# Performance work log

Measured on AMD Instinct MI355X. Metric: run time of the kernel, lower is better.

The kernel has to match this reference:

```python
import jax, jax.numpy as jnp
import numpy as np

B = 65536      # batch
IN = 784       # 1*28*28 flattened input
H = 768        # hidden_size
D = 3          # num_domains
E = 64         # expert hidden
C = 10         # classes
EPS = 1e-5     # BatchNorm eps


def setup_inputs() -> dict:
    key = jax.random.key(0)
    ks = jax.random.split(key, 8)
    s = lambda k, shp, sc: (jax.random.normal(k, shp, jnp.float32) * sc)
    return dict(
        x=jax.random.normal(ks[0], (B, 1, 28, 28), jnp.float32),
        # pre_classifier: Linear(784, H) + BatchNorm1d(H) affine params
        W1=s(ks[1], (IN, H), 0.03), b1=jnp.zeros((H,), jnp.float32),
        gamma=jnp.ones((H,), jnp.float32), beta=jnp.zeros((H,), jnp.float32),
        # discriminator: Linear(H,H) -> ReLU -> Linear(H,D)
        Wd1=s(ks[2], (H, H), 0.03), bd1=jnp.zeros((H,), jnp.float32),
        Wd2=s(ks[3], (H, D), 0.03), bd2=jnp.zeros((D,), jnp.float32),
        # per-domain expert classifiers: Linear(H,64) -> ReLU -> Linear(64,10), stacked over D
        Wa=s(ks[4], (D, H, E), 0.03), ba=jnp.zeros((D, E), jnp.float32),
        Wb=s(ks[5], (D, E, C), 0.1), bb=jnp.zeros((D, C), jnp.float32),
    )


def reference(x, W1, b1, gamma, beta, Wd1, bd1, Wd2, bd2, Wa, ba, Wb, bb):
    xf = x.reshape(x.shape[0], -1)                      # [B, 784]
    h = xf @ W1 + b1                                    # [B, H]
    # BatchNorm1d in training mode: batch mean / biased variance
    mu = h.mean(axis=0)
    var = jnp.mean((h - mu) ** 2, axis=0)
    feat = jax.nn.relu((h - mu) / jnp.sqrt(var + EPS) * gamma + beta)  # [B, H]
    # ReverseLayerF with alpha=0: identity forward, zero gradient back to feat
    rev = jax.lax.stop_gradient(feat)
    dom_out = jax.nn.relu(rev @ Wd1 + bd1) @ Wd2 + bd2  # [B, D]
    dom_pred = jnp.argmax(dom_out, axis=1)              # [B] int routing
    # hard routing: compute all D tiny experts densely, select by dom_pred
    hid = jax.nn.relu(jnp.einsum('bh,dhe->bde', feat, Wa) + ba)   # [B, D, E]
    all_out = jnp.einsum('bde,dec->bdc', hid, Wb) + bb            # [B, D, C]
    outs = jnp.take_along_axis(all_out, dom_pred[:, None, None], axis=1)[:, 0, :]  # [B, C]
    return outs, dom_out
```

## Files before the change

### kernel.cpp

```cpp
#include <hip/hip_runtime.h>
#include <math.h>

#define BATCH 65536
#define KIN   784
#define HD    768
#define FCAP  16384

typedef float f32x4 __attribute__((ext_vector_type(4)));
typedef short s16x8 __attribute__((ext_vector_type(8)));
typedef unsigned int __attribute__((address_space(3))) lds_u32;
typedef const unsigned int __attribute__((address_space(1))) glb_u32;

__device__ __forceinline__ float frelu(float x){ return x > 0.f ? x : 0.f; }

__device__ __forceinline__ unsigned int cvtpk(float a, float b){
    unsigned int r;
    asm("v_cvt_pk_bf16_f32 %0, %1, %2" : "=v"(r) : "v"(a), "v"(b));
    return r;
}
__device__ __forceinline__ unsigned short f2bf(float v){
    unsigned int u = __builtin_bit_cast(unsigned int, v);
    u += 0x7FFFu + ((u >> 16) & 1u);
    return (unsigned short)(u >> 16);
}
__device__ __forceinline__ float bf2f(unsigned short s){
    unsigned int u = ((unsigned int)s) << 16;
    return __builtin_bit_cast(float, u);
}
__device__ __forceinline__ void gload16(const void* g, void* l){
    __builtin_amdgcn_global_load_lds((glb_u32*)g, (lds_u32*)l, 16, 0, 0);
}

__global__ __launch_bounds__(256)
void cvtX(const float* __restrict__ x, unsigned short* __restrict__ xbf)
{
    int idx = blockIdx.x * 256 + threadIdx.x;
    int row = idx / 104, c = (idx - row * 104) * 8;
    uint4 o = make_uint4(0, 0, 0, 0);
    if (c < KIN) {
        const float* p = x + (size_t)row * KIN + c;
        float4 a = *(const float4*)p;
        float4 b = *(const float4*)(p + 4);
        o.x = cvtpk(a.x, a.y); o.y = cvtpk(a.z, a.w);
        o.z = cvtpk(b.x, b.y); o.w = cvtpk(b.z, b.w);
    }
    *(uint4*)(xbf + (size_t)row * 832 + c) = o;
}

__global__ __launch_bounds__(256)
void featBN(const unsigned short* __restrict__ hbf,
            const float* __restrict__ scale, const float* __restrict__ shift,
            unsigned short* __restrict__ fbf)
{
    int idx = blockIdx.x * 256 + threadIdx.x;
    int row = idx / 96, c = (idx - row * 96) * 8;
    s16x8 hv = *(const s16x8*)(hbf + (size_t)row * HD + c);
    float4 s0 = *(const float4*)(scale + c), s1 = *(const float4*)(scale + c + 4);
    float4 t0 = *(const float4*)(shift + c), t1 = *(const float4*)(shift + c + 4);
    float v[8];
    v[0] = frelu(bf2f((unsigned short)hv[0]) * s0.x + t0.x);
    v[1] = frelu(bf2f((unsigned short)hv[1]) * s0.y + t0.y);
    v[2] = frelu(bf2f((unsigned short)hv[2]) * s0.z + t0.z);
    v[3] = frelu(bf2f((unsigned short)hv[3]) * s0.w + t0.w);
    v[4] = frelu(bf2f((unsigned short)hv[4]) * s1.x + t1.x);
    v[5] = frelu(bf2f((unsigned short)hv[5]) * s1.y + t1.y);
    v[6] = frelu(bf2f((unsigned short)hv[6]) * s1.z + t1.z);
    v[7] = frelu(bf2f((unsigned short)hv[7]) * s1.w + t1.w);
    uint4 o;
    o.x = cvtpk(v[0], v[1]); o.y = cvtpk(v[2], v[3]);
    o.z = cvtpk(v[4], v[5]); o.w = cvtpk(v[6], v[7]);
    *(uint4*)(fbf + (size_t)row * HD + c) = o;
}

__global__ __launch_bounds__(256)
void tileW(const float* __restrict__ W, char* __restrict__ Wh, char* __restrict__ Wl,
           int K, int N, int NT)
{
    int chunk = blockIdx.x;
    int nb = chunk / NT, t = chunk - nb * NT;
    int tid = threadIdx.x;
    #pragma unroll
    for (int q = 0; q < 2; q++) {
        int idx = q * 256 + tid;
        int r = idx >> 2, p = idx & 3;
        int s = (p ^ ((r >> 1) & 3)) & 3;
        int kb = t * 32 + s * 8;
        int n = nb * 128 + r;
        s16x8 hv, lv;
        #pragma unroll
        for (int e = 0; e < 8; e++) {
            int k = kb + e;
            float v = (k < K) ? W[(size_t)k * N + n] : 0.f;
            unsigned short h = f2bf(v);
            hv[e] = (short)h;
            lv[e] = (short)f2bf(v - bf2f(h));
        }
        *(s16x8*)(Wh + (size_t)chunk * 8192 + idx * 16) = hv;
        *(s16x8*)(Wl + (size_t)chunk * 8192 + idx * 16) = lv;
    }
}

__global__ __launch_bounds__(256)
void tileWa(const float* __restrict__ Wa, char* __restrict__ WaC)
{
    int chunk = blockIdx.x;
    int d = chunk / 24, t = chunk - d * 24;
    int idx = threadIdx.x;
    int r = idx >> 2, p = idx & 3;
    int s = (p ^ ((r >> 1) & 3)) & 3;
    int kb = t * 32 + s * 8;
    s16x8 hv;
    #pragma unroll
    for (int e = 0; e < 8; e++)
        hv[e] = (short)f2bf(Wa[((size_t)d * HD + kb + e) * 64 + r]);
    *(s16x8*)(WaC + (size_t)chunk * 4096 + idx * 16) = hv;
}

template<int MODE>
__global__ __launch_bounds__(256, 3)
void gemm97(const unsigned short* __restrict__ Abf,
            const char* __restrict__ BhC,
            const float* __restrict__ bias,
            unsigned short* __restrict__ Hbf,
            const float* __restrict__ Wd2, double* __restrict__ domacc,
            float* __restrict__ sp1, float* __restrict__ sp2,
            int KP, int NT)
{
    __shared__ __align__(16) char sm[32768];

    int bid = blockIdx.x;
    int wg = (bid & 7) * 384 + (bid >> 3);
    int mb = wg / 6, nb = wg - mb * 6;
    int m0 = mb << 7, n0 = nb << 7;

    int tid = threadIdx.x;
    int lane = tid & 63, wid = tid >> 6;
    int wr = wid >> 1, wc = wid & 1;
    int l15 = lane & 15, l4 = lane >> 4;

    int aoff[4], boff[4];
    #pragma unroll
    for (int f = 0; f < 4; f++) {
        int ra = wr * 64 + f * 16 + l15;
        aoff[f] = ra * 64 + (((l4 ^ (ra >> 1)) & 3) << 4);
        int rb = wc * 64 + f * 16 + l15;
        boff[f] = rb * 64 + (((l4 ^ (rb >> 1)) & 3) << 4);
    }

    int ar[2], asl[2];
    #pragma unroll
    for (int q = 0; q < 2; q++) {
        int idx = q * 256 + tid;
        int r = idx >> 2, p = idx & 3;
        asl[q] = (p ^ ((r >> 1) & 3)) & 3;
        ar[q] = r;
    }

    f32x4 acc[4][4];
    #pragma unroll
    for (int i = 0; i < 4; i++)
        #pragma unroll
        for (int j = 0; j < 4; j++) acc[i][j] = (f32x4){0.f, 0.f, 0.f, 0.f};

    int NTc = 2 * NT;
    for (int t = 0; t < NT; t++) {
        int t2 = 2 * t;
        #pragma unroll
        for (int h = 0; h < 2; h++) {
            #pragma unroll
            for (int q = 0; q < 2; q++) {
                const unsigned short* src = Abf + (size_t)(m0 + ar[q]) * KP
                                          + (t2 + h) * 32 + asl[q] * 8;
                gload16(src, sm + h * 8192 + (q * 256 + tid) * 16);
            }
        }
        #pragma unroll
        for (int h = 0; h < 2; h++) {
            size_t cb = (size_t)(nb * NTc + t2 + h) * 8192;
            #pragma unroll
            for (int q = 0; q < 2; q++) {
                int off = (q * 256 + tid) * 16;
                gload16(BhC + cb + off, sm + 16384 + h * 8192 + off);
            }
        }
        __syncthreads();
        #pragma unroll
        for (int h = 0; h < 2; h++) {
            const char* ab  = sm + h * 8192;
            const char* bb2 = sm + 16384 + h * 8192;
            s16x8 fah[4], fbh[4];
            #pragma unroll
            for (int f = 0; f < 4; f++) {
                fah[f] = *(const s16x8*)(ab + aoff[f]);
                fbh[f] = *(const s16x8*)(bb2 + boff[f]);
            }
            #pragma unroll
            for (int i = 0; i < 4; i++)
                #pragma unroll
                for (int j = 0; j < 4; j++)
                    acc[i][j] = __builtin_amdgcn_mfma_f32_16x16x32_bf16(fah[i], fbh[j], acc[i][j], 0, 0, 0);
        }
        __syncthreads();
    }

    if (MODE == 0) {
        float bc[4];
        #pragma unroll
        for (int f = 0; f < 4; f++) bc[f] = bias[n0 + wc * 64 + f * 16 + l15];
        float cs[4] = {0.f,0.f,0.f,0.f}, cq[4] = {0.f,0.f,0.f,0.f};
        #pragma unroll
        for (int i = 0; i < 4; i++) {
            int rowb = m0 + wr * 64 + i * 16 + l4 * 4;
            #pragma unroll
            for (int j2 = 0; j2 < 4; j2++) {
                unsigned short* hrow = Hbf + (size_t)(rowb + j2) * HD + n0 + wc * 64 + l15;
                #pragma unroll
                for (int f = 0; f < 4; f++) {
                    float v = acc[i][f][j2] + bc[f];
                    hrow[f * 16] = (unsigned short)cvtpk(v, v);
                    cs[f] += v; cq[f] += v * v;
                }
            }
        }
        #pragma unroll
        for (int m = 16; m < 64; m <<= 1)
            #pragma unroll
            for (int f = 0; f < 4; f++) {
                cs[f] += __shfl_xor(cs[f], m, 64);
                cq[f] += __shfl_xor(cq[f], m, 64);
            }
        if (l4 == 0) {
            #pragma unroll
            for (int f = 0; f < 4; f++) {
                int col = n0 + wc * 64 + f * 16 + l15;
                sp1[(size_t)col * 1024 + mb * 2 + wr] = cs[f];
                sp2[(size_t)col * 1024 + mb * 2 + wr] = cq[f];
            }
        }
    } else {
        float bc[4], w2[4][3];
        #pragma unroll
        for (int f = 0; f < 4; f++) {
            int col = n0 + wc * 64 + f * 16 + l15;
            bc[f] = bias[col];
            w2[f][0] = Wd2[col * 3 + 0]; w2[f][1] = Wd2[col * 3 + 1]; w2[f][2] = Wd2[col * 3 + 2];
        }
        float s0[16], s1[16], s2[16];
        #pragma unroll
        for (int i = 0; i < 16; i++) { s0[i] = 0.f; s1[i] = 0.f; s2[i] = 0.f; }
        #pragma unroll
        for (int i = 0; i < 4; i++)
            #pragma unroll
            for (int j2 = 0; j2 < 4; j2++) {
                int idx = i * 4 + j2;
                #pragma unroll
                for (int f = 0; f < 4; f++) {
                    float v = frelu(acc[i][f][j2] + bc[f]);
                    s0[idx] += v * w2[f][0];
                    s1[idx] += v * w2[f][1];
                    s2[idx] += v * w2[f][2];
                }
            }
        #pragma unroll
        for (int m = 1; m < 16; m <<= 1) {
            #pragma unroll
            for (int i = 0; i < 16; i++) {
                s0[i] += __shfl_xor(s0[i], m, 64);
                s1[i] += __shfl_xor(s1[i], m, 64);
                s2[i] += __shfl_xor(s2[i], m, 64);
            }
        }
        if (l15 == 0) {
            #pragma unroll
            for (int i = 0; i < 16; i++) {
                int row = m0 + wr * 64 + (i >> 2) * 16 + l4 * 4 + (i & 3);
                atomicAdd(&domacc[(size_t)row * 3 + 0], (double)s0[i]);
                atomicAdd(&domacc[(size_t)row * 3 + 1], (double)s1[i]);
                atomicAdd(&domacc[(size_t)row * 3 + 2], (double)s2[i]);
            }
        }
    }
}

__global__ __launch_bounds__(256)
void bnfinal(const float* __restrict__ sp1, const float* __restrict__ sp2,
             const float* __restrict__ gamma, const float* __restrict__ beta,
             float* __restrict__ scale, float* __restrict__ shift)
{
    int c = blockIdx.x, t = threadIdx.x;
    const float* p1 = sp1 + (size_t)c * 1024;
    const float* p2 = sp2 + (size_t)c * 1024;
    double S = (double)p1[t] + (double)p1[t + 256] + (double)p1[t + 512] + (double)p1[t + 768];
    double Q = (double)p2[t] + (double)p2[t + 256] + (double)p2[t + 512] + (double)p2[t + 768];
    #pragma unroll
    for (int m = 1; m < 64; m <<= 1) { S += __shfl_xor(S, m, 64); Q += __shfl_xor(Q, m, 64); }
    __shared__ double sd1[4], sd2[4];
    int w = t >> 6;
    if ((t & 63) == 0) { sd1[w] = S; sd2[w] = Q; }
    __syncthreads();
    if (t == 0) {
        double Sa = sd1[0] + sd1[1] + sd1[2] + sd1[3];
        double Qa = sd2[0] + sd2[1] + sd2[2] + sd2[3];
        double mu  = Sa * (1.0 / 65536.0);
        double var = Qa * (1.0 / 65536.0) - mu * mu;
        double inv = 1.0 / sqrt(var + 1e-5);
        double sc  = inv * (double)gamma[c];
        double sh  = (double)beta[c] - mu * sc;
        scale[c] = (float)sc;
        shift[c] = (float)sh;
    }
}

__global__ __launch_bounds__(256)
void domfinal_a(const double* __restrict__ domacc, const float* __restrict__ bd2,
                float* __restrict__ outdom, int* __restrict__ fixmeta, int* __restrict__ fixlist)
{
    int r = blockIdx.x * 256 + threadIdx.x;
    double v0 = domacc[(size_t)r * 3 + 0] + (double)bd2[0];
    double v1 = domacc[(size_t)r * 3 + 1] + (double)bd2[1];
    double v2 = domacc[(size_t)r * 3 + 2] + (double)bd2[2];
    outdom[(size_t)r * 3 + 0] = (float)v0;
    outdom[(size_t)r * 3 + 1] = (float)v1;
    outdom[(size_t)r * 3 + 2] = (float)v2;
    double mx01 = v0 > v1 ? v0 : v1, mn01 = v0 > v1 ? v1 : v0;
    double best = mx01 > v2 ? mx01 : v2;
    double m2   = mx01 > v2 ? (mn01 > v2 ? mn01 : v2) : mx01;
    if (best - m2 < 1.5e-2) {
        int p = atomicAdd(fixmeta, 1);
        fixlist[p] = r;
    }
}

__global__ __launch_bounds__(256)
void gfix1(const int* __restrict__ fixmeta, const int* __restrict__ fixlist,
           const float* __restrict__ x,
           const char* __restrict__ BhC, const char* __restrict__ BlC,
           const float* __restrict__ b1, const float* __restrict__ scale,
           const float* __restrict__ shift,
           unsigned short* __restrict__ ffh, unsigned short* __restrict__ ffl)
{
    __shared__ __align__(16) char sm[32768];
    __shared__ int rowidx[128];
    int nfix = fixmeta[0]; if (nfix > FCAP) nfix = FCAP;
    int start = blockIdx.x * 128;
    if (start >= nfix) return;
    int nb = blockIdx.y;
    int n0 = nb << 7;

    int tid = threadIdx.x;
    int lane = tid & 63, wid = tid >> 6;
    int wr = wid >> 1, wc = wid & 1;
    int l15 = lane & 15, l4 = lane >> 4;

    if (tid < 128) {
        int i = start + tid;
        rowidx[tid] = fixlist[i < nfix ? i : nfix - 1];
    }
    __syncthreads();

    int aoff[4], boff[4];
    #pragma unroll
    for (int f = 0; f < 4; f++) {
        int ra = wr * 64 + f * 16 + l15;
        aoff[f] = ra * 64 + (((l4 ^ (ra >> 1)) & 3) << 4);
        int rb = wc * 64 + f * 16 + l15;
        boff[f] = rb * 64 + (((l4 ^ (rb >> 1)) & 3) << 4);
    }
    int ar[2], asl[2], arow[2];
    #pragma unroll
    for (int q = 0; q < 2; q++) {
        int idx = q * 256 + tid;
        int r = idx >> 2, p = idx & 3;
        asl[q] = (p ^ ((r >> 1) & 3)) & 3;
        ar[q] = r;
        arow[q] = rowidx[r];
    }

    f32x4 acc[4][4];
    #pragma unroll
    for (int i = 0; i < 4; i++)
        #pragma unroll
        for (int j = 0; j < 4; j++) acc[i][j] = (f32x4){0.f, 0.f, 0.f, 0.f};

    float av[2][8];
    auto loadA = [&](int t) {
        #pragma unroll
        for (int q = 0; q < 2; q++) {
            int kb = t * 32 + asl[q] * 8;
            const float* src = x + (size_t)arow[q] * KIN + kb;
            if (kb + 7 < KIN) {
                *(float4*)&av[q][0] = *(const float4*)src;
                *(float4*)&av[q][4] = *(const float4*)(src + 4);
            } else {
                #pragma unroll
                for (int e = 0; e < 8; e++) av[q][e] = (kb + e < KIN) ? src[e] : 0.f;
            }
        }
    };
    auto writeA = [&]() {
        #pragma unroll
        for (int q = 0; q < 2; q++) {
            int idx = q * 256 + tid;
            float* v = av[q];
            uint4 oh;
            oh.x = cvtpk(v[0], v[1]); oh.y = cvtpk(v[2], v[3]);
            oh.z = cvtpk(v[4], v[5]); oh.w = cvtpk(v[6], v[7]);
            float h0 = bf2f((unsigned short)(oh.x & 0xFFFF));
            float h1 = bf2f((unsigned short)(oh.x >> 16));
            float h2 = bf2f((unsigned short)(oh.y & 0xFFFF));
            float h3 = bf2f((unsigned short)(oh.y >> 16));
            float h4 = bf2f((unsigned short)(oh.z & 0xFFFF));
            float h5 = bf2f((unsigned short)(oh.z >> 16));
            float h6 = bf2f((unsigned short)(oh.w & 0xFFFF));
            float h7 = bf2f((unsigned short)(oh.w >> 16));
            uint4 ol;
            ol.x = cvtpk(v[0] - h0, v[1] - h1); ol.y = cvtpk(v[2] - h2, v[3] - h3);
            ol.z = cvtpk(v[4] - h4, v[5] - h5); ol.w = cvtpk(v[6] - h6, v[7] - h7);
            *(uint4*)(sm + idx * 16) = oh;
            *(uint4*)(sm + 8192 + idx * 16) = ol;
        }
    };

    loadA(0);
    const int NTc = 26;
    for (int t = 0; t < NTc; t++) {
        __syncthreads();
        size_t cb = (size_t)(nb * NTc + t) * 8192;
        #pragma unroll
        for (int q = 0; q < 2; q++) {
            int off = (q * 256 + tid) * 16;
            gload16(BhC + cb + off, sm + 16384 + off);
            gload16(BlC + cb + off, sm + 24576 + off);
        }
        writeA();
        if (t + 1 < NTc) loadA(t + 1);
        __syncthreads();
        s16x8 fah[4], fal[4], fbh[4], fbl[4];
        #pragma unroll
        for (int f = 0; f < 4; f++) {
            fah[f] = *(const s16x8*)(sm + aoff[f]);
            fal[f] = *(const s16x8*)(sm + 8192 + aoff[f]);
            fbh[f] = *(const s16x8*)(sm + 16384 + boff[f]);
            fbl[f] = *(const s16x8*)(sm + 24576 + boff[f]);
        }
        #pragma unroll
        for (int i = 0; i < 4; i++)
            #pragma unroll
            for (int j = 0; j < 4; j++) {
                acc[i][j] = __builtin_amdgcn_mfma_f32_16x16x32_bf16(fah[i], fbl[j], acc[i][j], 0, 0, 0);
                acc[i][j] = __builtin_amdgcn_mfma_f32_16x16x32_bf16(fal[i], fbh[j], acc[i][j], 0, 0, 0);
                acc[i][j] = __builtin_amdgcn_mfma_f32_16x16x32_bf16(fah[i], fbh[j], acc[i][j], 0, 0, 0);
            }
    }

    float bc[4], sc[4], sh[4];
    #pragma unroll
    for (int f = 0; f < 4; f++) {
        int col = n0 + wc * 64 + f * 16 + l15;
        bc[f] = b1[col]; sc[f] = scale[col]; sh[f] = shift[col];
    }
    #pragma unroll
    for (int i = 0; i < 4; i++) {
        #pragma unroll
        for (int j2 = 0; j2 < 4; j2++) {
            int pos = start + wr * 64 + i * 16 + l4 * 4 + j2;
            if (pos < nfix) {
                #pragma unroll
                for (int f = 0; f < 4; f++) {
                    int col = n0 + wc * 64 + f * 16 + l15;
                    float fl = frelu((acc[i][f][j2] + bc[f]) * sc[f] + sh[f]);
                    unsigned short hi = (unsigned short)cvtpk(fl, fl);
                    unsigned short lo = (unsigned short)cvtpk(fl - bf2f(hi), 0.f);
                    ffh[(size_t)pos * HD + col] = hi;
                    ffl[(size_t)pos * HD + col] = lo;
                }
            }
        }
    }
}

__global__ __launch_bounds__(256)
void gfix2(const int* __restrict__ fixmeta,
           const unsigned short* __restrict__ ffh, const unsigned short* __restrict__ ffl,
           const char* __restrict__ BhC, const char* __restrict__ BlC,
           const float* __restrict__ bd1, const float* __restrict__ Wd2,
           double* __restrict__ domfix)
{
    __shared__ __align__(16) char sm[32768];
    int nfix = fixmeta[0]; if (nfix > FCAP) nfix = FCAP;
    int start = blockIdx.x * 128;
    if (start >= nfix) return;
    int nb = blockIdx.y;
    int n0 = nb << 7;

    int tid = threadIdx.x;
    int lane = tid & 63, wid = tid >> 6;
    int wr = wid >> 1, wc = wid & 1;
    int l15 = lane & 15, l4 = lane >> 4;

    int aoff[4], boff[4];
    #pragma unroll
    for (int f = 0; f < 4; f++) {
        int ra = wr * 64 + f * 16 + l15;
        aoff[f] = ra * 64 + (((l4 ^ (ra >> 1)) & 3) << 4);
        int rb = wc * 64 + f * 16 + l15;
        boff[f] = rb * 64 + (((l4 ^ (rb >> 1)) & 3) << 4);
    }
    int arow[2], asl[2];
    #pragma unroll
    for (int q = 0; q < 2; q++) {
        int idx = q * 256 + tid;
        int r = idx >> 2, p = idx & 3;
        asl[q] = (p ^ ((r >> 1) & 3)) & 3;
        int pos = start + r;
        arow[q] = pos < nfix ? pos : nfix - 1;
    }

    f32x4 acc[4][4];
    #pragma unroll
    for (int i = 0; i < 4; i++)
        #pragma unroll
        for (int j = 0; j < 4; j++) acc[i][j] = (f32x4){0.f, 0.f, 0.f, 0.f};

    const int NTc = 24;
    for (int t = 0; t < NTc; t++) {
        #pragma unroll
        for (int q = 0; q < 2; q++) {
            size_t ao = (size_t)arow[q] * HD + t * 32 + asl[q] * 8;
            gload16(ffh + ao, sm + (q * 256 + tid) * 16);
            gload16(ffl + ao, sm + 8192 + (q * 256 + tid) * 16);
        }
        size_t cb = (size_t)(nb * NTc + t) * 8192;
        #pragma unroll
        for (int q = 0; q < 2; q++) {
            int off = (q * 256 + tid) * 16;
            gload16(BhC + cb + off, sm + 16384 + off);
            gload16(BlC + cb + off, sm + 24576 + off);
        }
        __syncthreads();
        s16x8 fah[4], fal[4], fbh[4], fbl[4];
        #pragma unroll
        for (int f = 0; f < 4; f++) {
            fah[f] = *(const s16x8*)(sm + aoff[f]);
            fal[f] = *(const s16x8*)(sm + 8192 + aoff[f]);
            fbh[f] = *(const s16x8*)(sm + 16384 + boff[f]);
            fbl[f] = *(const s16x8*)(sm + 24576 + boff[f]);
        }
        #pragma unroll
        for (int i = 0; i < 4; i++)
            #pragma unroll
            for (int j = 0; j < 4; j++) {
                acc[i][j] = __builtin_amdgcn_mfma_f32_16x16x32_bf16(fah[i], fbl[j], acc[i][j], 0, 0, 0);
                acc[i][j] = __builtin_amdgcn_mfma_f32_16x16x32_bf16(fal[i], fbh[j], acc[i][j], 0, 0, 0);
                acc[i][j] = __builtin_amdgcn_mfma_f32_16x16x32_bf16(fah[i], fbh[j], acc[i][j], 0, 0, 0);
            }
        __syncthreads();
    }

    float bc[4], w2[4][3];
    #pragma unroll
    for (int f = 0; f < 4; f++) {
        int col = n0 + wc * 64 + f * 16 + l15;
        bc[f] = bd1[col];
        w2[f][0] = Wd2[col * 3 + 0]; w2[f][1] = Wd2[col * 3 + 1]; w2[f][2] = Wd2[col * 3 + 2];
    }
    float s0[16], s1[16], s2[16];
    #pragma unroll
    for (int i = 0; i < 16; i++) { s0[i] = 0.f; s1[i] = 0.f; s2[i] = 0.f; }
    #pragma unroll
    for (int i = 0; i < 4; i++)
        #pragma unroll
        for (int j2 = 0; j2 < 4; j2++) {
            int idx = i * 4 + j2;
            #pragma unroll
            for (int f = 0; f < 4; f++) {
                float v = frelu(acc[i][f][j2] + bc[f]);
                s0[idx] += v * w2[f][0];
                s1[idx] += v * w2[f][1];
                s2[idx] += v * w2[f][2];
            }
        }
    #pragma unroll
    for (int m = 1; m < 16; m <<= 1) {
        #pragma unroll
        for (int i = 0; i < 16; i++) {
            s0[i] += __shfl_xor(s0[i], m, 64);
            s1[i] += __shfl_xor(s1[i], m, 64);
            s2[i] += __shfl_xor(s2[i], m, 64);
        }
    }
    if (l15 == 0) {
        #pragma unroll
        for (int i = 0; i < 16; i++) {
            int pos = start + wr * 64 + (i >> 2) * 16 + l4 * 4 + (i & 3);
            if (pos < nfix) {
                atomicAdd(&domfix[(size_t)pos * 3 + 0], (double)s0[i]);
                atomicAdd(&domfix[(size_t)pos * 3 + 1], (double)s1[i]);
                atomicAdd(&domfix[(size_t)pos * 3 + 2], (double)s2[i]);
            }
        }
    }
}

__global__ __launch_bounds__(256)
void fixfin(const int* __restrict__ fixmeta, const int* __restrict__ fixlist,
            const double* __restrict__ domfix, const float* __restrict__ bd2,
            float* __restrict__ outdom)
{
    int nfix = fixmeta[0]; if (nfix > FCAP) nfix = FCAP;
    int i = blockIdx.x * 256 + threadIdx.x;
    if (i < nfix) {
        int row = fixlist[i];
        outdom[(size_t)row * 3 + 0] = (float)(domfix[(size_t)i * 3 + 0] + (double)bd2[0]);
        outdom[(size_t)row * 3 + 1] = (float)(domfix[(size_t)i * 3 + 1] + (double)bd2[1]);
        outdom[(size_t)row * 3 + 2] = (float)(domfix[(size_t)i * 3 + 2] + (double)bd2[2]);
    }
}

__global__ __launch_bounds__(256)
void domfinal_b(const float* __restrict__ outdom, int* __restrict__ cnt, int* __restrict__ lists)
{
    __shared__ int lcnt[3], base[3];
    int tid = threadIdx.x;
    if (tid < 3) lcnt[tid] = 0;
    __syncthreads();
    int r = blockIdx.x * 256 + tid;
    float v0 = outdom[(size_t)r * 3 + 0];
    float v1 = outdom[(size_t)r * 3 + 1];
    float v2 = outdom[(size_t)r * 3 + 2];
    int p = 0; float best = v0;
    if (v1 > best) { best = v1; p = 1; }
    if (v2 > best) { best = v2; p = 2; }
    int lpos = atomicAdd(&lcnt[p], 1);
    __syncthreads();
    if (tid < 3) base[tid] = atomicAdd(&cnt[tid], lcnt[tid]);
    __syncthreads();
    lists[(size_t)p * BATCH + base[p] + lpos] = r;
}

__global__ __launch_bounds__(256)
void expert_mfma(const unsigned short* __restrict__ fbf,
                 const char* __restrict__ WaC,
                 const int* __restrict__ cnt, const int* __restrict__ lists,
                 const float* __restrict__ ba,
                 const float* __restrict__ Wb, const float* __restrict__ bb,
                 float* __restrict__ outs)
{
    __shared__ __align__(16) char sm[12288];
    __shared__ float hid[128][66];
    __shared__ int rowidx[128];

    int d = blockIdx.y;
    int count = cnt[d];
    int start = blockIdx.x * 128;
    if (start >= count) return;
    int nrows = count - start; if (nrows > 128) nrows = 128;

    int tid = threadIdx.x;
    int lane = tid & 63, wid = tid >> 6;
    int l15 = lane & 15, l4 = lane >> 4;

    if (tid < 128) {
        int i = tid < nrows ? tid : nrows - 1;
        rowidx[tid] = lists[(size_t)d * BATCH + start + i];
    }
    __syncthreads();

    int asl[2], arow[2];
    #pragma unroll
    for (int q = 0; q < 2; q++) {
        int idx = q * 256 + tid;
        int r = idx >> 2, p = idx & 3;
        asl[q] = (p ^ ((r >> 1) & 3)) & 3;
        arow[q] = rowidx[r];
    }

    int aoff[2], boff[4];
    #pragma unroll
    for (int i2 = 0; i2 < 2; i2++) {
        int ra = wid * 32 + i2 * 16 + l15;
        aoff[i2] = ra * 64 + (((l4 ^ (ra >> 1)) & 3) << 4);
    }
    #pragma unroll
    for (int f = 0; f < 4; f++) {
        int rb = f * 16 + l15;
        boff[f] = rb * 64 + (((l4 ^ (rb >> 1)) & 3) << 4);
    }

    f32x4 acc[2][4];
    #pragma unroll
    for (int i = 0; i < 2; i++)
        #pragma unroll
        for (int j = 0; j < 4; j++) acc[i][j] = (f32x4){0.f, 0.f, 0.f, 0.f};

    for (int t = 0; t < 24; t++) {
        #pragma unroll
        for (int q = 0; q < 2; q++)
            gload16(fbf + (size_t)arow[q] * HD + t * 32 + asl[q] * 8,
                    sm + (q * 256 + tid) * 16);
        gload16(WaC + (size_t)(d * 24 + t) * 4096 + tid * 16, sm + 8192 + tid * 16);
        __syncthreads();
        s16x8 fa[2], fb[4];
        #pragma unroll
        for (int i2 = 0; i2 < 2; i2++) fa[i2] = *(const s16x8*)(sm + aoff[i2]);
        #pragma unroll
        for (int f = 0; f < 4; f++)    fb[f]  = *(const s16x8*)(sm + 8192 + boff[f]);
        #pragma unroll
        for (int i2 = 0; i2 < 2; i2++)
            #pragma unroll
            for (int f = 0; f < 4; f++)
                acc[i2][f] = __builtin_amdgcn_mfma_f32_16x16x32_bf16(fa[i2], fb[f], acc[i2][f], 0, 0, 0);
        __syncthreads();
    }

    #pragma unroll
    for (int i2 = 0; i2 < 2; i2++)
        #pragma unroll
        for (int f = 0; f < 4; f++) {
            int col = f * 16 + l15;
            float bav = ba[d * 64 + col];
            #pragma unroll
            for (int j = 0; j < 4; j++) {
                int row = wid * 32 + i2 * 16 + l4 * 4 + j;
                hid[row][col] = frelu(acc[i2][f][j] + bav);
            }
        }
    __syncthreads();

    for (int o = tid; o < 1280; o += 256) {
        int r2 = o / 10, c = o - r2 * 10;
        if (r2 < nrows) {
            float s = 0.f;
            #pragma unroll 16
            for (int l = 0; l < 64; l++) s += hid[r2][l] * Wb[((size_t)d * 64 + l) * 10 + c];
            outs[(size_t)rowidx[r2] * 10 + c] = s + bb[d * 10 + c];
        }
    }
}

extern "C" void kernel_launch(void* const* d_in, const int* in_sizes, int n_in,
                              void* d_out, int out_size, void* d_ws, size_t ws_size,
                              hipStream_t stream)
{
    const float* x     = (const float*)d_in[0];
    const float* W1    = (const float*)d_in[1];
    const float* b1    = (const float*)d_in[2];
    const float* gamma = (const float*)d_in[3];
    const float* beta  = (const float*)d_in[4];
    const float* Wd1   = (const float*)d_in[5];
    const float* bd1   = (const float*)d_in[6];
    const float* Wd2   = (const float*)d_in[7];
    const float* bd2   = (const float*)d_in[8];
    const float* Wa    = (const float*)d_in[9];
    const float* ba    = (const float*)d_in[10];
    const float* Wb    = (const float*)d_in[11];
    const float* bb    = (const float*)d_in[12];

    float* out    = (float*)d_out;
    float* outs   = out;
    float* outdom = out + (size_t)BATCH * 10;

    const int NT1 = 13, NT2 = 12;
    const int NTC1 = 26, NTC2 = 24;

    char* ws = (char*)d_ws;
    size_t off = 0;
    unsigned short* hbf = (unsigned short*)(ws + off); off += (size_t)BATCH * HD * 2;
    unsigned short* xbf = (unsigned short*)(ws + off); off += (size_t)BATCH * 832 * 2;
    unsigned short* fbf = xbf;
    unsigned short* ffh = hbf;
    unsigned short* ffl = hbf + (size_t)FCAP * HD;
    char*  W1hC   = ws + off;            off += (size_t)6 * NTC1 * 8192;
    char*  W1loC  = ws + off;            off += (size_t)6 * NTC1 * 8192;
    char*  Wd1hC  = ws + off;            off += (size_t)6 * NTC2 * 8192;
    char*  Wd1loC = ws + off;            off += (size_t)6 * NTC2 * 8192;
    char*  WaC    = ws + off;            off += (size_t)3 * 24 * 4096;
    float* sp1    = (float*)(ws + off);  off += (size_t)HD * 1024 * 4;
    float* sp2    = (float*)(ws + off);  off += (size_t)HD * 1024 * 4;
    float* scale  = (float*)(ws + off);  off += HD * 4;
    float* shift  = (float*)(ws + off);  off += HD * 4;
    size_t zoff = off;
    double* domacc = (double*)(ws + off); off += (size_t)BATCH * 3 * 8;
    double* domfix = (double*)(ws + off); off += (size_t)FCAP * 3 * 8;
    int*    cnt    = (int*)(ws + off);    off += 64;
    int*    fixmeta= (int*)(ws + off);    off += 64;
    size_t zbytes = off - zoff;
    int*    lists  = (int*)(ws + off);    off += (size_t)3 * BATCH * 4;
    int*    fixlist= (int*)(ws + off);    off += (size_t)BATCH * 4;

    hipMemsetAsync(ws + zoff, 0, zbytes, stream);

    tileW<<<6 * NTC1, 256, 0, stream>>>(W1, W1hC, W1loC, KIN, HD, NTC1);
    tileW<<<6 * NTC2, 256, 0, stream>>>(Wd1, Wd1hC, Wd1loC, HD, HD, NTC2);
    tileWa<<<72, 256, 0, stream>>>(Wa, WaC);
    cvtX<<<BATCH * 104 / 256, 256, 0, stream>>>(x, xbf);

    gemm97<0><<<3072, 256, 0, stream>>>(xbf, W1hC, b1, hbf,
                                        nullptr, nullptr, sp1, sp2, 832, NT1);
    bnfinal<<<HD, 256, 0, stream>>>(sp1, sp2, gamma, beta, scale, shift);
    featBN<<<BATCH * 96 / 256, 256, 0, stream>>>(hbf, scale, shift, fbf);
    gemm97<1><<<3072, 256, 0, stream>>>(fbf, Wd1hC, bd1, nullptr,
                                        Wd2, domacc, nullptr, nullptr, HD, NT2);
    domfinal_a<<<BATCH / 256, 256, 0, stream>>>(domacc, bd2, outdom, fixmeta, fixlist);
    {
        dim3 fg(FCAP / 128, 6);
        gfix1<<<fg, 256, 0, stream>>>(fixmeta, fixlist, x, W1hC, W1loC,
                                      b1, scale, shift, ffh, ffl);
        gfix2<<<fg, 256, 0, stream>>>(fixmeta, ffh, ffl, Wd1hC, Wd1loC,
                                      bd1, Wd2, domfix);
        fixfin<<<FCAP / 256, 256, 0, stream>>>(fixmeta, fixlist, domfix, bd2, outdom);
    }
    domfinal_b<<<BATCH / 256, 256, 0, stream>>>(outdom, cnt, lists);
    dim3 eg(512, 3);
    expert_mfma<<<eg, 256, 0, stream>>>(fbf, WaC, cnt, lists, ba, Wb, bb, outs);
}
```

Baseline: 573.2 us.

## Widen GEMM block tile to 128x256 with 8 waves sharing the A tile

Both main GEMM launches now use 512-thread blocks covering 128 rows by 256 columns, instead of 256-thread blocks covering 128x128. The A tile loaded into LDS is shared across two 128-column B chunks, which halves global A traffic and the number of blocks. LDS per block grows to 48KB and the min-blocks-per-CU hint is dropped. This can lower occupancy and change register allocation. The epilogue must stay consistent with the new wave-to-column mapping.

Result: slower. 589.3 us (+2.8%).

```diff
diff --git a/kernel.cpp b/kernel.cpp
--- a/kernel.cpp
+++ b/kernel.cpp
@@ -117,7 +117,7 @@
 }
 
 template<int MODE>
-__global__ __launch_bounds__(256, 3)
+__global__ __launch_bounds__(512)
 void gemm97(const unsigned short* __restrict__ Abf,
             const char* __restrict__ BhC,
             const float* __restrict__ bias,
@@ -126,16 +126,16 @@
             float* __restrict__ sp1, float* __restrict__ sp2,
             int KP, int NT)
 {
-    __shared__ __align__(16) char sm[32768];
+    __shared__ __align__(16) char sm[49152];
 
     int bid = blockIdx.x;
-    int wg = (bid & 7) * 384 + (bid >> 3);
-    int mb = wg / 6, nb = wg - mb * 6;
-    int m0 = mb << 7, n0 = nb << 7;
+    int wg = (bid & 7) * 192 + (bid >> 3);
+    int mb = wg / 3, ct = wg - mb * 3;
+    int m0 = mb << 7, n0 = ct << 8;
 
     int tid = threadIdx.x;
     int lane = tid & 63, wid = tid >> 6;
-    int wr = wid >> 1, wc = wid & 1;
+    int wr = wid >> 2, wc = wid & 3;
     int l15 = lane & 15, l4 = lane >> 4;
 
     int aoff[4], boff[4];
@@ -143,17 +143,16 @@
     for (int f = 0; f < 4; f++) {
         int ra = wr * 64 + f * 16 + l15;
         aoff[f] = ra * 64 + (((l4 ^ (ra >> 1)) & 3) << 4);
-        int rb = wc * 64 + f * 16 + l15;
-        boff[f] = rb * 64 + (((l4 ^ (rb >> 1)) & 3) << 4);
-    }
-
-    int ar[2], asl[2];
-    #pragma unroll
-    for (int q = 0; q < 2; q++) {
-        int idx = q * 256 + tid;
-        int r = idx >> 2, p = idx & 3;
-        asl[q] = (p ^ ((r >> 1) & 3)) & 3;
-        ar[q] = r;
+        int cc = wc >> 1, sub = wc & 1;
+        int rb = sub * 64 + f * 16 + l15;
+        boff[f] = cc * 8192 + rb * 64 + (((l4 ^ (rb >> 1)) & 3) << 4);
+    }
+
+    int ar, asl;
+    {
+        int r = tid >> 2, p = tid & 3;
+        asl = (p ^ ((r >> 1) & 3)) & 3;
+        ar = r;
     }
 
     f32x4 acc[4][4];
@@ -167,27 +166,23 @@
         int t2 = 2 * t;
         #pragma unroll
         for (int h = 0; h < 2; h++) {
-            #pragma unroll
-            for (int q = 0; q < 2; q++) {
-                const unsigned short* src = Abf + (size_t)(m0 + ar[q]) * KP
-                                          + (t2 + h) * 32 + asl[q] * 8;
-                gload16(src, sm + h * 8192 + (q * 256 + tid) * 16);
-            }
-        }
-        #pragma unroll
-        for (int h = 0; h < 2; h++) {
-            size_t cb = (size_t)(nb * NTc + t2 + h) * 8192;
-            #pragma unroll
-            for (int q = 0; q < 2; q++) {
-                int off = (q * 256 + tid) * 16;
-                gload16(BhC + cb + off, sm + 16384 + h * 8192 + off);
-            }
-        }
+            const unsigned short* src = Abf + (size_t)(m0 + ar) * KP
+                                      + (t2 + h) * 32 + asl * 8;
+            gload16(src, sm + h * 8192 + tid * 16);
+        }
+        #pragma unroll
+        for (int h = 0; h < 2; h++)
+            #pragma unroll
+            for (int cc = 0; cc < 2; cc++) {
+                size_t cb = (size_t)((2 * ct + cc) * NTc + t2 + h) * 8192;
+                gload16(BhC + cb + tid * 16,
+                        sm + 16384 + h * 16384 + cc * 8192 + tid * 16);
+            }
         __syncthreads();
         #pragma unroll
         for (int h = 0; h < 2; h++) {
             const char* ab  = sm + h * 8192;
-            const char* bb2 = sm + 16384 + h * 8192;
+            const char* bb2 = sm + 16384 + h * 16384;
             s16x8 fah[4], fbh[4];
             #pragma unroll
             for (int f = 0; f < 4; f++) {
@@ -795,11 +790,11 @@
     tileWa<<<72, 256, 0, stream>>>(Wa, WaC);
     cvtX<<<BATCH * 104 / 256, 256, 0, stream>>>(x, xbf);
 
-    gemm97<0><<<3072, 256, 0, stream>>>(xbf, W1hC, b1, hbf,
+    gemm97<0><<<1536, 512, 0, stream>>>(xbf, W1hC, b1, hbf,
                                         nullptr, nullptr, sp1, sp2, 832, NT1);
     bnfinal<<<HD, 256, 0, stream>>>(sp1, sp2, gamma, beta, scale, shift);
     featBN<<<BATCH * 96 / 256, 256, 0, stream>>>(hbf, scale, shift, fbf);
-    gemm97<1><<<3072, 256, 0, stream>>>(fbf, Wd1hC, bd1, nullptr,
+    gemm97<1><<<1536, 512, 0, stream>>>(fbf, Wd1hC, bd1, nullptr,
                                         Wd2, domacc, nullptr, nullptr, HD, NT2);
     domfinal_a<<<BATCH / 256, 256, 0, stream>>>(domacc, bd2, outdom, fixmeta, fixlist);
     {
```
